# Performance work log

Measured on AMD Instinct MI355X. Metric: run time of the kernel, lower is better.

## Reference

```python
import jax, jax.numpy as jnp
import numpy as np

N_SETS, N_POINTS, D_FEAT = 8, 4096, 16
K = 16


def setup_inputs() -> dict:
    key = jax.random.key(0)
    x = jax.random.normal(key, (N_SETS, N_POINTS, D_FEAT), dtype=jnp.float32)
    return {"x": x, "k": K}


def reference(x, k):
    """Faithful kNN-graph construction.

    x: (N, M, D) point sets. Returns (src, dst) flattened edge lists with
    per-sample node-ID offsets (node j of set i -> global id i*M + j), plus
    the top-k squared distances (the selection values).
    """
    n_samples, n_points, _ = x.shape
    # pairwise squared distance: ||xi||^2 + ||xj||^2 - 2 xi.xj  -> (N, M, M)
    x2s = jnp.sum(x * x, axis=-1, keepdims=True)
    dist = x2s + jnp.swapaxes(x2s, -1, -2) - 2.0 * jnp.einsum("nmd,npd->nmp", x, x)
    # k smallest distances per row (argtopk descending=False)
    neg_vals, k_indices = jax.lax.top_k(-dist, k)            # (N, M, k)
    topk_dist = -neg_vals
    per_sample_offset = (jnp.arange(n_samples, dtype=jnp.int32) * n_points)[:, None, None]
    dst = k_indices.astype(jnp.int32) + per_sample_offset     # neighbor ids
    src = jnp.broadcast_to(
        jnp.arange(n_points, dtype=jnp.int32)[None, :, None], k_indices.shape
    ) + per_sample_offset                                     # query ids
    return src.reshape(-1), dst.reshape(-1), topk_dist
```

## Files before the change

### kernel.cpp

```cpp
#include <hip/hip_runtime.h>
#include <hip/hip_bf16.h>

#define NSETS 8
#define NPTS  4096
#define DF    16
#define KNN   16
#define QPB   64
#define NCH   8
#define BLK   (QPB * NCH)
#define CHUNK (NPTS / NCH)
#define NEDGE (NSETS * NPTS * KNN)

#define RES      15
#define FLUSH_AT 12
#define GRP      4

__global__ __launch_bounds__(BLK) void knn_kernel(const float* __restrict__ x,
                                                  float* __restrict__ out) {
    __shared__ float nrm[NPTS];
    __shared__ float tau_sh[QPB];
    __shared__ __align__(16) char smem[RES * BLK * 8];
    float2*         resv  = (float2*)smem;
    float*          lds_d = (float*)smem;
    unsigned short* lds_i = (unsigned short*)(smem + BLK * KNN * 4);

    const int t    = threadIdx.x;
    const int lane = t & 63;
    const int wv   = t >> 6;
    const int set  = blockIdx.x >> 6;
    const int q0   = (blockIdx.x & 63) * QPB;
    const int q    = q0 + lane;

    const float* xs = x + (size_t)set * NPTS * DF;

    if (t < QPB) tau_sh[t] = 3.0e38f;

    for (int r = 0; r < NPTS / BLK; ++r) {
        const int c = r * BLK + t;
        const float4* p = (const float4*)(xs + (size_t)c * DF);
        float4 a = p[0], b = p[1], g = p[2], d = p[3];
        float r0 = __fadd_rn(__fmul_rn(a.x, a.x), __fmul_rn(g.x, g.x));
        float r1 = __fadd_rn(__fmul_rn(a.y, a.y), __fmul_rn(g.y, g.y));
        float r2 = __fadd_rn(__fmul_rn(a.z, a.z), __fmul_rn(g.z, g.z));
        float r3 = __fadd_rn(__fmul_rn(a.w, a.w), __fmul_rn(g.w, g.w));
        float r4 = __fadd_rn(__fmul_rn(b.x, b.x), __fmul_rn(d.x, d.x));
        float r5 = __fadd_rn(__fmul_rn(b.y, b.y), __fmul_rn(d.y, d.y));
        float r6 = __fadd_rn(__fmul_rn(b.z, b.z), __fmul_rn(d.z, d.z));
        float r7 = __fadd_rn(__fmul_rn(b.w, b.w), __fmul_rn(d.w, d.w));
        nrm[c] = __fadd_rn(
            __fadd_rn(__fadd_rn(r0, r1), __fadd_rn(r2, r3)),
            __fadd_rn(__fadd_rn(r4, r5), __fadd_rn(r6, r7)));
    }
    __syncthreads();

    float qn[DF];
    {
        const float4* qp = (const float4*)(xs + (size_t)q * DF);
        float4 v0 = qp[0], v1 = qp[1], v2 = qp[2], v3 = qp[3];
        qn[0]=v0.x; qn[1]=v0.y; qn[2]=v0.z; qn[3]=v0.w;
        qn[4]=v1.x; qn[5]=v1.y; qn[6]=v1.z; qn[7]=v1.w;
        qn[8]=v2.x; qn[9]=v2.y; qn[10]=v2.z; qn[11]=v2.w;
        qn[12]=v3.x; qn[13]=v3.y; qn[14]=v3.z; qn[15]=v3.w;
    }
    const float q2 = nrm[q];
#pragma unroll
    for (int d = 0; d < DF; ++d) qn[d] = -2.0f * qn[d];

    float Ld[KNN];
    int   Li[KNN];
#pragma unroll
    for (int j = 0; j < KNN; ++j) { Ld[j] = 3.0e38f; Li[j] = 0; }
    int cnt = 0;

    const int cb = __builtin_amdgcn_readfirstlane(wv * CHUNK);

    auto flush = [&]() {
        for (int e = 0; e < RES; ++e) {
            if (!__any(e < cnt)) break;
            float2 en = resv[e * BLK + t];
            const float d  = (e < cnt) ? en.x : 3.0e38f;
            const int   ci = __float_as_int(en.y);
            if (d < Ld[KNN - 1]) {
#pragma unroll
                for (int j = KNN - 1; j >= 1; --j) {
                    const bool sh   = d < Ld[j - 1];
                    const bool here = d < Ld[j];
                    const float nd = sh ? Ld[j - 1] : (here ? d  : Ld[j]);
                    const int   ni = sh ? Li[j - 1] : (here ? ci : Li[j]);
                    Ld[j] = nd; Li[j] = ni;
                }
                if (d < Ld[0]) { Ld[0] = d; Li[0] = ci; }
            }
        }
        cnt = 0;
        volatile float* ts = (volatile float*)tau_sh;
        float cur = ts[lane];
        ts[lane] = fminf(cur, Ld[KNN - 1]);
    };

    for (int g = 0; g < CHUNK; g += GRP) {
        const float tsh = ((volatile float*)tau_sh)[lane];
        const float tau = fminf(tsh, Ld[KNN - 1]);
#pragma unroll
        for (int u = 0; u < GRP; ++u) {
            const int c = cb + g + u;
            const float* cf = xs + (size_t)c * DF;
            float dot = 0.f;
#pragma unroll
            for (int d = 0; d < DF; ++d) dot = fmaf(qn[d], cf[d], dot);
            const float dist = __fadd_rn(__fadd_rn(q2, nrm[c]), dot);
            if (dist <= tau) {
                resv[cnt * BLK + t] = make_float2(dist, __int_as_float(c));
                ++cnt;
            }
        }
        if (__any(cnt >= FLUSH_AT)) flush();
    }
    flush();

    __syncthreads();
#pragma unroll
    for (int j = 0; j < KNN; ++j) {
        lds_d[t * KNN + j] = Ld[j];
        lds_i[t * KNN + j] = (unsigned short)Li[j];
    }
    __syncthreads();

    if (t < QPB) {
        const int l = t;
        float h[NCH];
        int   p[NCH];
#pragma unroll
        for (int w2 = 0; w2 < NCH; ++w2) {
            p[w2] = 0;
            h[w2] = lds_d[(w2 * QPB + l) * KNN];
        }

        const int    gq = set * NPTS + q0 + l;
        const size_t eb = (size_t)gq * KNN;
        float* osrc = out;
        float* odst = out + (size_t)NEDGE;
        float* odis = out + 2 * (size_t)NEDGE;
        const float srcf = (float)gq;

        for (int e = 0; e < KNN; ++e) {
            float best = h[0];
            int   bw   = 0;
#pragma unroll
            for (int w2 = 1; w2 < NCH; ++w2)
                if (h[w2] < best) { best = h[w2]; bw = w2; }
            int li = 0;
#pragma unroll
            for (int w2 = 0; w2 < NCH; ++w2) {
                if (bw == w2) {
                    li = (int)lds_i[(w2 * QPB + l) * KNN + p[w2]];
                    ++p[w2];
                    h[w2] = (p[w2] < KNN) ? lds_d[(w2 * QPB + l) * KNN + p[w2]]
                                          : 3.0e38f;
                }
            }

            osrc[eb + e] = srcf;
            odst[eb + e] = (float)(set * NPTS + li);
            odis[eb + e] = best;
        }
    }
}

extern "C" void kernel_launch(void* const* d_in, const int* in_sizes, int n_in,
                              void* d_out, int out_size, void* d_ws, size_t ws_size,
                              hipStream_t stream) {
    (void)in_sizes; (void)n_in; (void)out_size; (void)d_ws; (void)ws_size;
    const float* x = (const float*)d_in[0];
    float* out = (float*)d_out;

    knn_kernel<<<NSETS * (NPTS / QPB), BLK, 0, stream>>>(x, out);
}
```

Measured before the change: 241.8 us.

## Stage candidate tiles in LDS and interleave candidates across waves per tile

Replaces per-wave contiguous chunks read from global memory with 512-point tiles cooperatively loaded into LDS (features plus norms), which each wave then scans as a slice per tile. Candidate features now come from LDS as float4 reads instead of scalar global loads, and norms are computed per tile rather than for the whole set up front. The reservoir is shrunk (RES 8, flush at 5) to fit the LDS budget, which means more frequent flushes. The final merge also adds index tie-breaking, and each tile load adds two block-wide barriers.

```diff
diff --git a/kernel.cpp b/kernel.cpp
--- a/kernel.cpp
+++ b/kernel.cpp
@@ -8,19 +8,27 @@
 #define QPB   64
 #define NCH   8
 #define BLK   (QPB * NCH)
-#define CHUNK (NPTS / NCH)
+#define TILE  512
+#define NTILE (NPTS / TILE)
+#define SLICE (TILE / NCH)
 #define NEDGE (NSETS * NPTS * KNN)
 
-#define RES      15
-#define FLUSH_AT 12
+#define RES      8
+#define FLUSH_AT 5
 #define GRP      4
+
+#define FEAT_B   (TILE * DF * 4)
+#define NRM_B    (TILE * 4)
+#define RESV_OFF (FEAT_B + NRM_B)
+#define SMEM_B   (RESV_OFF + RES * BLK * 8)
 
 __global__ __launch_bounds__(BLK) void knn_kernel(const float* __restrict__ x,
                                                   float* __restrict__ out) {
-    __shared__ float nrm[NPTS];
     __shared__ float tau_sh[QPB];
-    __shared__ __align__(16) char smem[RES * BLK * 8];
-    float2*         resv  = (float2*)smem;
+    __shared__ __align__(16) char smem[SMEM_B];
+    float4* feat4 = (float4*)smem;
+    float*  nrm_t = (float*)(smem + FEAT_B);
+    float2* resv  = (float2*)(smem + RESV_OFF);
     float*          lds_d = (float*)smem;
     unsigned short* lds_i = (unsigned short*)(smem + BLK * KNN * 4);
 
@@ -35,10 +43,11 @@
 
     if (t < QPB) tau_sh[t] = 3.0e38f;
 
-    for (int r = 0; r < NPTS / BLK; ++r) {
-        const int c = r * BLK + t;
-        const float4* p = (const float4*)(xs + (size_t)c * DF);
-        float4 a = p[0], b = p[1], g = p[2], d = p[3];
+    float qn[DF];
+    float q2;
+    {
+        const float4* qp = (const float4*)(xs + (size_t)q * DF);
+        float4 a = qp[0], b = qp[1], g = qp[2], d = qp[3];
         float r0 = __fadd_rn(__fmul_rn(a.x, a.x), __fmul_rn(g.x, g.x));
         float r1 = __fadd_rn(__fmul_rn(a.y, a.y), __fmul_rn(g.y, g.y));
         float r2 = __fadd_rn(__fmul_rn(a.z, a.z), __fmul_rn(g.z, g.z));
@@ -47,32 +56,21 @@
         float r5 = __fadd_rn(__fmul_rn(b.y, b.y), __fmul_rn(d.y, d.y));
         float r6 = __fadd_rn(__fmul_rn(b.z, b.z), __fmul_rn(d.z, d.z));
         float r7 = __fadd_rn(__fmul_rn(b.w, b.w), __fmul_rn(d.w, d.w));
-        nrm[c] = __fadd_rn(
-            __fadd_rn(__fadd_rn(r0, r1), __fadd_rn(r2, r3)),
-            __fadd_rn(__fadd_rn(r4, r5), __fadd_rn(r6, r7)));
-    }
-    __syncthreads();
-
-    float qn[DF];
-    {
-        const float4* qp = (const float4*)(xs + (size_t)q * DF);
-        float4 v0 = qp[0], v1 = qp[1], v2 = qp[2], v3 = qp[3];
-        qn[0]=v0.x; qn[1]=v0.y; qn[2]=v0.z; qn[3]=v0.w;
-        qn[4]=v1.x; qn[5]=v1.y; qn[6]=v1.z; qn[7]=v1.w;
-        qn[8]=v2.x; qn[9]=v2.y; qn[10]=v2.z; qn[11]=v2.w;
-        qn[12]=v3.x; qn[13]=v3.y; qn[14]=v3.z; qn[15]=v3.w;
-    }
-    const float q2 = nrm[q];
-#pragma unroll
-    for (int d = 0; d < DF; ++d) qn[d] = -2.0f * qn[d];
+        q2 = __fadd_rn(__fadd_rn(__fadd_rn(r0, r1), __fadd_rn(r2, r3)),
+                       __fadd_rn(__fadd_rn(r4, r5), __fadd_rn(r6, r7)));
+        qn[0]=a.x; qn[1]=a.y; qn[2]=a.z; qn[3]=a.w;
+        qn[4]=b.x; qn[5]=b.y; qn[6]=b.z; qn[7]=b.w;
+        qn[8]=g.x; qn[9]=g.y; qn[10]=g.z; qn[11]=g.w;
+        qn[12]=d.x; qn[13]=d.y; qn[14]=d.z; qn[15]=d.w;
+#pragma unroll
+        for (int d2 = 0; d2 < DF; ++d2) qn[d2] = -2.0f * qn[d2];
+    }
 
     float Ld[KNN];
     int   Li[KNN];
 #pragma unroll
     for (int j = 0; j < KNN; ++j) { Ld[j] = 3.0e38f; Li[j] = 0; }
     int cnt = 0;
-
-    const int cb = __builtin_amdgcn_readfirstlane(wv * CHUNK);
 
     auto flush = [&]() {
         for (int e = 0; e < RES; ++e) {
@@ -98,23 +96,62 @@
         ts[lane] = fminf(cur, Ld[KNN - 1]);
     };
 
-    for (int g = 0; g < CHUNK; g += GRP) {
-        const float tsh = ((volatile float*)tau_sh)[lane];
-        const float tau = fminf(tsh, Ld[KNN - 1]);
-#pragma unroll
-        for (int u = 0; u < GRP; ++u) {
-            const int c = cb + g + u;
-            const float* cf = xs + (size_t)c * DF;
-            float dot = 0.f;
-#pragma unroll
-            for (int d = 0; d < DF; ++d) dot = fmaf(qn[d], cf[d], dot);
-            const float dist = __fadd_rn(__fadd_rn(q2, nrm[c]), dot);
-            if (dist <= tau) {
-                resv[cnt * BLK + t] = make_float2(dist, __int_as_float(c));
-                ++cnt;
-            }
-        }
-        if (__any(cnt >= FLUSH_AT)) flush();
+    for (int tile = 0; tile < NTILE; ++tile) {
+        __syncthreads();
+        {
+            const int c = tile * TILE + t;
+            const float4* p = (const float4*)(xs + (size_t)c * DF);
+            float4 a = p[0], b = p[1], g = p[2], d = p[3];
+            float r0 = __fadd_rn(__fmul_rn(a.x, a.x), __fmul_rn(g.x, g.x));
+            float r1 = __fadd_rn(__fmul_rn(a.y, a.y), __fmul_rn(g.y, g.y));
+            float r2 = __fadd_rn(__fmul_rn(a.z, a.z), __fmul_rn(g.z, g.z));
+            float r3 = __fadd_rn(__fmul_rn(a.w, a.w), __fmul_rn(g.w, g.w));
+            float r4 = __fadd_rn(__fmul_rn(b.x, b.x), __fmul_rn(d.x, d.x));
+            float r5 = __fadd_rn(__fmul_rn(b.y, b.y), __fmul_rn(d.y, d.y));
+            float r6 = __fadd_rn(__fmul_rn(b.z, b.z), __fmul_rn(d.z, d.z));
+            float r7 = __fadd_rn(__fmul_rn(b.w, b.w), __fmul_rn(d.w, d.w));
+            feat4[0 * TILE + t] = a;
+            feat4[1 * TILE + t] = b;
+            feat4[2 * TILE + t] = g;
+            feat4[3 * TILE + t] = d;
+            nrm_t[t] = __fadd_rn(
+                __fadd_rn(__fadd_rn(r0, r1), __fadd_rn(r2, r3)),
+                __fadd_rn(__fadd_rn(r4, r5), __fadd_rn(r6, r7)));
+        }
+        __syncthreads();
+
+        const int lbase = wv * SLICE;
+        const int gbase = tile * TILE + lbase;
+
+        for (int g = 0; g < SLICE; g += GRP) {
+            const float tsh = ((volatile float*)tau_sh)[lane];
+            const float tau = fminf(tsh, Ld[KNN - 1]);
+#pragma unroll
+            for (int u = 0; u < GRP; ++u) {
+                const int lc = lbase + g + u;
+                float4 f0 = feat4[0 * TILE + lc];
+                float4 f1 = feat4[1 * TILE + lc];
+                float4 f2 = feat4[2 * TILE + lc];
+                float4 f3 = feat4[3 * TILE + lc];
+                const float nc = nrm_t[lc];
+                float dot = 0.f;
+                dot = fmaf(qn[0],  f0.x, dot); dot = fmaf(qn[1],  f0.y, dot);
+                dot = fmaf(qn[2],  f0.z, dot); dot = fmaf(qn[3],  f0.w, dot);
+                dot = fmaf(qn[4],  f1.x, dot); dot = fmaf(qn[5],  f1.y, dot);
+                dot = fmaf(qn[6],  f1.z, dot); dot = fmaf(qn[7],  f1.w, dot);
+                dot = fmaf(qn[8],  f2.x, dot); dot = fmaf(qn[9],  f2.y, dot);
+                dot = fmaf(qn[10], f2.z, dot); dot = fmaf(qn[11], f2.w, dot);
+                dot = fmaf(qn[12], f3.x, dot); dot = fmaf(qn[13], f3.y, dot);
+                dot = fmaf(qn[14], f3.z, dot); dot = fmaf(qn[15], f3.w, dot);
+                const float dist = __fadd_rn(__fadd_rn(q2, nc), dot);
+                if (dist <= tau) {
+                    resv[cnt * BLK + t] =
+                        make_float2(dist, __int_as_float(gbase + g + u));
+                    ++cnt;
+                }
+            }
+            if (__any(cnt >= FLUSH_AT)) flush();
+        }
     }
     flush();
 
@@ -129,11 +166,13 @@
     if (t < QPB) {
         const int l = t;
         float h[NCH];
+        int   hi[NCH];
         int   p[NCH];
 #pragma unroll
         for (int w2 = 0; w2 < NCH; ++w2) {
-            p[w2] = 0;
-            h[w2] = lds_d[(w2 * QPB + l) * KNN];
+            p[w2]  = 0;
+            h[w2]  = lds_d[(w2 * QPB + l) * KNN];
+            hi[w2] = (int)lds_i[(w2 * QPB + l) * KNN];
         }
 
         const int    gq = set * NPTS + q0 + l;
@@ -145,23 +184,31 @@
 
         for (int e = 0; e < KNN; ++e) {
             float best = h[0];
+            int   bi   = hi[0];
             int   bw   = 0;
 #pragma unroll
-            for (int w2 = 1; w2 < NCH; ++w2)
-                if (h[w2] < best) { best = h[w2]; bw = w2; }
-            int li = 0;
+            for (int w2 = 1; w2 < NCH; ++w2) {
+                const bool better = (h[w2] < best) ||
+                                    (h[w2] == best && hi[w2] < bi);
+                if (better) { best = h[w2]; bi = hi[w2]; bw = w2; }
+            }
+
 #pragma unroll
             for (int w2 = 0; w2 < NCH; ++w2) {
                 if (bw == w2) {
-                    li = (int)lds_i[(w2 * QPB + l) * KNN + p[w2]];
                     ++p[w2];
-                    h[w2] = (p[w2] < KNN) ? lds_d[(w2 * QPB + l) * KNN + p[w2]]
-                                          : 3.0e38f;
+                    if (p[w2] < KNN) {
+                        h[w2]  = lds_d[(w2 * QPB + l) * KNN + p[w2]];
+                        hi[w2] = (int)lds_i[(w2 * QPB + l) * KNN + p[w2]];
+                    } else {
+                        h[w2]  = 3.0e38f;
+                        hi[w2] = 0x7FFFFFFF;
+                    }
                 }
             }
 
             osrc[eb + e] = srcf;
-            odst[eb + e] = (float)(set * NPTS + li);
+            odst[eb + e] = (float)(set * NPTS + bi);
             odis[eb + e] = best;
         }
     }
```

Measured after the change: 229.2 us. -5.2%, faster.
